# Performance work log

Hardware: AMD Instinct MI355X
Metric: run time of the kernel (lower is better)

The kernel has to match this reference:

```python
import jax, jax.numpy as jnp
import numpy as np

B, S, D = 8, 2048, 768
H = 4 * D  # MLP hidden
EPS = 1e-5


def setup_inputs() -> dict:
    key = jax.random.key(0)
    ks = jax.random.split(key, 12)
    sd = 1.0 / np.sqrt(D)
    sh = 1.0 / np.sqrt(H)
    return {
        "x": jax.random.normal(ks[0], (B, S, D), dtype=jnp.float32),
        "ln1_g": jnp.ones((D,), jnp.float32),
        "ln1_b": jnp.zeros((D,), jnp.float32),
        "ln2_g": jnp.ones((D,), jnp.float32),
        "ln2_b": jnp.zeros((D,), jnp.float32),
        "Wq": jax.random.normal(ks[1], (D, D), jnp.float32) * sd,
        "bq": jnp.zeros((D,), jnp.float32),
        "Wk": jax.random.normal(ks[2], (D, D), jnp.float32) * sd,
        "bk": jnp.zeros((D,), jnp.float32),
        "Wv": jax.random.normal(ks[3], (D, D), jnp.float32) * sd,
        "bv": jnp.zeros((D,), jnp.float32),
        "Wo": jax.random.normal(ks[4], (D, D), jnp.float32) * sd,
        "bo": jnp.zeros((D,), jnp.float32),
        "Wfc": jax.random.normal(ks[5], (D, H), jnp.float32) * sd,
        "bfc": jnp.zeros((H,), jnp.float32),
        "Wproj": jax.random.normal(ks[6], (H, D), jnp.float32) * sh,
        "bproj": jnp.zeros((D,), jnp.float32),
    }


def _layernorm(x, g, b):
    mu = jnp.mean(x, axis=-1, keepdims=True)
    var = jnp.mean(jnp.square(x - mu), axis=-1, keepdims=True)
    return (x - mu) * jax.lax.rsqrt(var + EPS) * g + b


def reference(x, ln1_g, ln1_b, ln2_g, ln2_b, Wq, bq, Wk, bk, Wv, bv, Wo, bo,
              Wfc, bfc, Wproj, bproj):
    d = x.shape[-1]
    # --- attention sub-block (single head, full D) ---
    h = _layernorm(x, ln1_g, ln1_b)
    q = h @ Wq + bq            # [B,S,D]
    k = h @ Wk + bk
    v = h @ Wv + bv
    scores = jnp.einsum("bsd,btd->bst", q, k) / jnp.sqrt(jnp.float32(d))
    attn = jax.nn.softmax(scores, axis=-1)  # softmax over keys (dim=2)
    y = jnp.einsum("bst,btd->bsd", attn, v)
    x = x + (y @ Wo + bo)
    # --- MLP sub-block (exact GELU like nn.GELU default) ---
    h2 = _layernorm(x, ln2_g, ln2_b)
    m = jax.nn.gelu(h2 @ Wfc + bfc, approximate=False)
    x = x + (m @ Wproj + bproj)  # dropout p=0 -> identity
    return x
```

## Files before the change

### kernel.cpp

```cpp
#include <hip/hip_runtime.h>
#include <hip/hip_bf16.h>

typedef __attribute__((ext_vector_type(8))) short short8;
typedef __attribute__((ext_vector_type(4))) float floatx4;

using bf16 = __hip_bfloat16;

__device__ __forceinline__ void cp16_g2l(bf16* lds_p, const bf16* g) {
  __builtin_amdgcn_global_load_lds(
      (const __attribute__((address_space(1))) unsigned int*)g,
      (__attribute__((address_space(3))) unsigned int*)lds_p,
      16, 0, 0);
}

__device__ __forceinline__ float gelu_exact(float x) {
  return 0.5f * x * (1.0f + erff(x * 0.70710678118654752f));
}

template<int MODE>
__global__ __launch_bounds__(256)
void gemm_bt(const bf16* __restrict__ A, long sAb, long lda,
             const bf16* __restrict__ Bt, long sBb, long ldb,
             const float* __restrict__ bias,
             const float* __restrict__ resid,
             float* __restrict__ rsum, long rsS, long cbStr,
             void* __restrict__ out, long sOb,
             int N, int K, float scale)
{
  constexpr bool PA = (MODE == 5);

  __shared__ __attribute__((aligned(16))) bf16 sA[3][128 * 32];
  __shared__ __attribute__((aligned(16))) bf16 sB[3][128 * 32];

  const int tid = threadIdx.x;
  const int l = tid & 63, w = tid >> 6;
  const int bz = blockIdx.z;
  const long row0 = (long)blockIdx.x * 128;
  const long col0 = (long)blockIdx.y * 128;

  const bf16* Ab = A + (long)bz * sAb;
  const bf16* Bb = Bt + (long)bz * sBb;

  const int sr = (w << 4) + (l >> 2);
  const int slot = (l & 3) ^ ((sr >> 1) & 3);
  const int kcd = (l & 3) << 3;
  const bf16* gA;
  long skipA, koA;
  if constexpr (PA) {
    gA    = Ab + ((long)(slot >> 1) * lda + row0 + sr) * 16 + ((slot & 1) << 3);
    skipA = 64 * 16;
    koA   = 32 * lda;
  } else {
    gA    = Ab + (row0 + sr) * lda + (slot << 3);
    skipA = 64 * lda;
    koA   = 32;
  }
  const bf16* gB = Bb + (col0 + sr) * ldb + (slot << 3);
  const long skipB = 64 * ldb;
  const int lofs = sr * 32 + kcd;

  floatx4 acc[4][4];
  #pragma unroll
  for (int i = 0; i < 4; ++i)
    #pragma unroll
    for (int j = 0; j < 4; ++j)
      acc[i][j] = (floatx4){0.f, 0.f, 0.f, 0.f};

  const int wr = (w >> 1) & 1, wc = w & 1;
  const int g = l >> 4, t = l & 15;
  const int swz = (g ^ ((t >> 1) & 3)) << 3;
  const int aoff = (wr * 64 + t) * 32 + swz;
  const int boff = (wc * 64 + t) * 32 + swz;

  const int nt = K >> 5;

  cp16_g2l(&sA[0][lofs],           gA);
  cp16_g2l(&sA[0][lofs] + 64 * 32, gA + skipA);
  cp16_g2l(&sB[0][lofs],           gB);
  cp16_g2l(&sB[0][lofs] + 64 * 32, gB + skipB);

  int bufc = 0;
  for (int kt = 0; kt < nt; ++kt) {
    const int nxtb = (bufc == 2) ? 0 : bufc + 1;
    if (kt + 1 < nt) {
      const long oA = (long)(kt + 1) * koA;
      const long oB = (long)(kt + 1) << 5;
      cp16_g2l(&sA[nxtb][lofs],           gA + oA);
      cp16_g2l(&sA[nxtb][lofs] + 64 * 32, gA + oA + skipA);
      cp16_g2l(&sB[nxtb][lofs],           gB + oB);
      cp16_g2l(&sB[nxtb][lofs] + 64 * 32, gB + oB + skipB);
      asm volatile("s_waitcnt vmcnt(4)" ::: "memory");
    } else {
      asm volatile("s_waitcnt vmcnt(0)" ::: "memory");
    }
    asm volatile("s_barrier" ::: "memory");

    const bf16* cA = &sA[bufc][0];
    const bf16* cB = &sB[bufc][0];
    short8 a[4], b[4];
    #pragma unroll
    for (int m = 0; m < 4; ++m) a[m] = *(const short8*)(cA + aoff + m * 512);
    #pragma unroll
    for (int n = 0; n < 4; ++n) b[n] = *(const short8*)(cB + boff + n * 512);
    #pragma unroll
    for (int m = 0; m < 4; ++m)
      #pragma unroll
      for (int n = 0; n < 4; ++n)
        acc[m][n] = __builtin_amdgcn_mfma_f32_16x16x32_bf16(a[m], b[n], acc[m][n], 0, 0, 0);
    bufc = nxtb;
  }

  const long orow = row0 + wr * 64 + (g << 2);
  const long ocol = col0 + wc * 64 + t;

  if constexpr (MODE == 0 || MODE == 4) {
    bf16* O = (bf16*)out + (long)bz * sOb;
    float bv4[4];
    #pragma unroll
    for (int n = 0; n < 4; ++n) bv4[n] = bias[ocol + n * 16];
    #pragma unroll
    for (int m = 0; m < 4; ++m) {
      #pragma unroll
      for (int r = 0; r < 4; ++r) {
        bf16* Or = O + (orow + m * 16 + r) * (long)N + ocol;
        #pragma unroll
        for (int n = 0; n < 4; ++n) {
          float vv = acc[m][n][r] + bv4[n];
          if constexpr (MODE == 4) vv = gelu_exact(vv);
          Or[n * 16] = __float2bfloat16(vv);
        }
      }
    }
  } else if constexpr (MODE == 3) {
    float* O = (float*)out;
    float bv4[4];
    #pragma unroll
    for (int n = 0; n < 4; ++n) bv4[n] = bias[ocol + n * 16];
    #pragma unroll
    for (int m = 0; m < 4; ++m) {
      #pragma unroll
      for (int r = 0; r < 4; ++r) {
        const long rb = (orow + m * 16 + r) * (long)N + ocol;
        #pragma unroll
        for (int n = 0; n < 4; ++n)
          O[rb + n * 16] = acc[m][n][r] + bv4[n] + resid[rb + n * 16];
      }
    }
  } else if constexpr (MODE == 5) {
    bf16* O = (bf16*)out + (long)bz * sOb;
    #pragma unroll
    for (int m = 0; m < 4; ++m) {
      #pragma unroll
      for (int r = 0; r < 4; ++r) {
        const long rr = orow + m * 16 + r;
        const float inv = 1.0f / rsum[bz * rsS + rr];
        bf16* Or = O + rr * (long)N + ocol;
        #pragma unroll
        for (int n = 0; n < 4; ++n)
          Or[n * 16] = __float2bfloat16(acc[m][n][r] * inv);
      }
    }
  } else {
    bf16* O = (bf16*)out + (long)bz * sOb;
    const long pb = (col0 >> 4) + wc * 4;
    float prow[4][4];
    #pragma unroll
    for (int m = 0; m < 4; ++m)
      #pragma unroll
      for (int r = 0; r < 4; ++r) prow[m][r] = 0.f;
    #pragma unroll
    for (int n = 0; n < 4; ++n) {
      bf16* Opan = O + (pb + n) * (rsS * 16) + t;
      #pragma unroll
      for (int m = 0; m < 4; ++m) {
        #pragma unroll
        for (int r = 0; r < 4; ++r) {
          const float p = __expf(acc[m][n][r] * scale);
          Opan[(orow + m * 16 + r) * 16] = __float2bfloat16(p);
          prow[m][r] += p;
        }
      }
    }
    #pragma unroll
    for (int m = 0; m < 4; ++m) {
      #pragma unroll
      for (int r = 0; r < 4; ++r) {
        float s = prow[m][r];
        s += __shfl_xor(s, 1);
        s += __shfl_xor(s, 2);
        s += __shfl_xor(s, 4);
        s += __shfl_xor(s, 8);
        if (t == 0)
          rsum[(long)(blockIdx.y * 2 + wc) * cbStr + bz * rsS +
               orow + m * 16 + r] = s;
      }
    }
  }
}

__global__ __launch_bounds__(256)
void reduce32(const float* __restrict__ rp, float* __restrict__ rs, int n)
{
  const int i = threadIdx.x + blockIdx.x * 256;
  if (i < n) {
    float s = 0.f;
    #pragma unroll
    for (int c = 0; c < 32; ++c) s += rp[(long)c * 16384 + i];
    rs[i] = s;
  }
}

__global__ __launch_bounds__(256)
void ln_kernel(const float* __restrict__ X, const float* __restrict__ G,
               const float* __restrict__ Bv, bf16* __restrict__ H)
{
  const int tid = threadIdx.x;
  const long row = blockIdx.x;
  const float* xr = X + row * 768;
  const float v0 = xr[tid], v1 = xr[tid + 256], v2 = xr[tid + 512];
  float s = v0 + v1 + v2;
  float s2 = v0 * v0 + v1 * v1 + v2 * v2;
  #pragma unroll
  for (int o = 32; o > 0; o >>= 1) {
    s += __shfl_xor(s, o);
    s2 += __shfl_xor(s2, o);
  }
  __shared__ float red[8];
  const int w = tid >> 6, l = tid & 63;
  if (l == 0) { red[w] = s; red[w + 4] = s2; }
  __syncthreads();
  s = red[0] + red[1] + red[2] + red[3];
  s2 = red[4] + red[5] + red[6] + red[7];
  const float mu = s * (1.f / 768.f);
  const float var = s2 * (1.f / 768.f) - mu * mu;
  const float rstd = rsqrtf(var + 1e-5f);
  bf16* hr = H + row * 768;
  hr[tid]       = __float2bfloat16((v0 - mu) * rstd * G[tid]       + Bv[tid]);
  hr[tid + 256] = __float2bfloat16((v1 - mu) * rstd * G[tid + 256] + Bv[tid + 256]);
  hr[tid + 512] = __float2bfloat16((v2 - mu) * rstd * G[tid + 512] + Bv[tid + 512]);
}

__global__ void transpose_w(const float* __restrict__ W, bf16* __restrict__ Wt,
                            int K, int N)
{
  __shared__ float tile[32][33];
  const int n0 = blockIdx.x * 32, k0 = blockIdx.y * 32;
  const int tx = threadIdx.x, ty = threadIdx.y;
  #pragma unroll
  for (int j = ty; j < 32; j += 8)
    tile[j][tx] = W[(long)(k0 + j) * N + n0 + tx];
  __syncthreads();
  #pragma unroll
  for (int j = ty; j < 32; j += 8)
    Wt[(long)(n0 + j) * K + k0 + tx] = __float2bfloat16(tile[tx][j]);
}

__global__ void transpose_v(const bf16* __restrict__ QKV, bf16* __restrict__ Vt)
{
  __shared__ bf16 tile[32][33];
  const int d0 = blockIdx.x * 32, s0 = blockIdx.y * 32, b = blockIdx.z;
  const int tx = threadIdx.x, ty = threadIdx.y;
  #pragma unroll
  for (int j = ty; j < 32; j += 8)
    tile[j][tx] = QKV[((long)b * 2048 + s0 + j) * 2304 + 1536 + d0 + tx];
  __syncthreads();
  #pragma unroll
  for (int j = ty; j < 32; j += 8)
    Vt[(long)b * 768 * 2048 + (long)(d0 + j) * 2048 + s0 + tx] = tile[tx][j];
}

__global__ void concat3(const float* __restrict__ a, const float* __restrict__ b,
                        const float* __restrict__ c, float* __restrict__ o)
{
  const int i = threadIdx.x + blockIdx.x * 256;
  if (i < 768) { o[i] = a[i]; o[i + 768] = b[i]; o[i + 1536] = c[i]; }
}

extern "C" void kernel_launch(void* const* d_in, const int* in_sizes, int n_in,
                              void* d_out, int out_size, void* d_ws, size_t ws_size,
                              hipStream_t stream)
{
  const float* x     = (const float*)d_in[0];
  const float* ln1g  = (const float*)d_in[1];
  const float* ln1b  = (const float*)d_in[2];
  const float* ln2g  = (const float*)d_in[3];
  const float* ln2b  = (const float*)d_in[4];
  const float* Wq    = (const float*)d_in[5];
  const float* bq    = (const float*)d_in[6];
  const float* Wk    = (const float*)d_in[7];
  const float* bk    = (const float*)d_in[8];
  const float* Wv    = (const float*)d_in[9];
  const float* bvv   = (const float*)d_in[10];
  const float* Wo    = (const float*)d_in[11];
  const float* bo    = (const float*)d_in[12];
  const float* Wfc   = (const float*)d_in[13];
  const float* bfc   = (const float*)d_in[14];
  const float* Wproj = (const float*)d_in[15];
  const float* bproj = (const float*)d_in[16];
  float* out = (float*)d_out;

  constexpr int Bz = 8, S = 2048, D = 768, Hh = 3072, QKVN = 3 * D;
  constexpr long Mtot = (long)Bz * S;

  char* ws = (char*)d_ws;
  size_t off = 0;
  auto alloc = [&](size_t bytes) -> char* {
    char* p = ws + off;
    off += (bytes + 255) & ~(size_t)255;
    return p;
  };
  bf16* wqkvT = (bf16*)alloc((size_t)QKVN * D * 2);
  bf16* woT   = (bf16*)alloc((size_t)D * D * 2);
  bf16* wfcT  = (bf16*)alloc((size_t)Hh * D * 2);
  bf16* wprT  = (bf16*)alloc((size_t)D * Hh * 2);
  float* bqkv = (float*)alloc((size_t)QKVN * 4);
  float* rsum = (float*)alloc((size_t)Mtot * 4);
  float* rpart= (float*)alloc((size_t)32 * Mtot * 4);
  bf16* hb    = (bf16*)alloc((size_t)Mtot * D * 2);
  bf16* qkv   = (bf16*)alloc((size_t)Mtot * QKVN * 2);
  bf16* vtb   = (bf16*)alloc((size_t)Mtot * D * 2);
  bf16* yb    = (bf16*)alloc((size_t)Mtot * D * 2);

  int nbat = Bz;
  size_t region = (size_t)nbat * S * S * 2;
  const size_t mbytes = (size_t)Mtot * Hh * 2;
  if (region < mbytes) region = mbytes;
  if (off + region > ws_size) {
    nbat = 1;
    region = mbytes;
  }
  char* reg = alloc(region);
  bf16* attn = (bf16*)reg;
  bf16* mb = (bf16*)reg;

  const dim3 tb(32, 8);

  transpose_w<<<dim3(D / 32, D / 32), tb, 0, stream>>>(Wq, wqkvT, D, D);
  transpose_w<<<dim3(D / 32, D / 32), tb, 0, stream>>>(Wk, wqkvT + (size_t)D * D, D, D);
  transpose_w<<<dim3(D / 32, D / 32), tb, 0, stream>>>(Wv, wqkvT + 2 * (size_t)D * D, D, D);
  transpose_w<<<dim3(D / 32, D / 32), tb, 0, stream>>>(Wo, woT, D, D);
  transpose_w<<<dim3(Hh / 32, D / 32), tb, 0, stream>>>(Wfc, wfcT, D, Hh);
  transpose_w<<<dim3(D / 32, Hh / 32), tb, 0, stream>>>(Wproj, wprT, Hh, D);
  concat3<<<3, 256, 0, stream>>>(bq, bk, bvv, bqkv);

  ln_kernel<<<(int)Mtot, 256, 0, stream>>>(x, ln1g, ln1b, hb);

  gemm_bt<0><<<dim3(Mtot / 128, QKVN / 128, 1), 256, 0, stream>>>(
      hb, 0, D, wqkvT, 0, D, bqkv, nullptr, nullptr, 0, 0, qkv, 0, QKVN, D, 1.f);
  transpose_v<<<dim3(D / 32, S / 32, Bz), tb, 0, stream>>>(qkv, vtb);

  const float sc = 0.03608439182435161f;
  for (int g0 = 0; g0 < Bz; g0 += nbat) {
    const bf16* qg  = qkv + (long)g0 * S * QKVN;
    const bf16* kg  = qkv + (long)g0 * S * QKVN + D;
    const bf16* vtg = vtb + (long)g0 * D * S;
    float* rsg = rsum + (long)g0 * S;
    float* rpg = rpart + (long)g0 * S;
    bf16* yg = yb + (long)g0 * S * D;
    gemm_bt<6><<<dim3(S / 128, S / 128, nbat), 256, 0, stream>>>(
        qg, (long)S * QKVN, QKVN, kg, (long)S * QKVN, QKVN, nullptr, nullptr,
        rpg, S, Mtot, attn, (long)S * S, S, D, sc);
    reduce32<<<(int)(Mtot / 256), 256, 0, stream>>>(rpart, rsum, (int)Mtot);
    gemm_bt<5><<<dim3(S / 128, D / 128, nbat), 256, 0, stream>>>(
        attn, (long)S * S, S, vtg, (long)D * S, S, nullptr, nullptr,
        rsg, S, 0, yg, (long)S * D, D, S, 1.f);
  }

  gemm_bt<3><<<dim3(Mtot / 128, D / 128, 1), 256, 0, stream>>>(
      yb, 0, D, woT, 0, D, bo, x, nullptr, 0, 0, out, 0, D, D, 1.f);

  ln_kernel<<<(int)Mtot, 256, 0, stream>>>(out, ln2g, ln2b, hb);

  gemm_bt<4><<<dim3(Mtot / 128, Hh / 128, 1), 256, 0, stream>>>(
      hb, 0, D, wfcT, 0, D, bfc, nullptr, nullptr, 0, 0, mb, 0, Hh, D, 1.f);
  gemm_bt<3><<<dim3(Mtot / 128, D / 128, 1), 256, 0, stream>>>(
      mb, 0, Hh, wprT, 0, Hh, bproj, out, nullptr, 0, 0, out, 0, D, Hh, 1.f);
}
```

Measured before the change: 625.6 us.

## Compute softmax row sums via ones-MFMA, remap workgroups, store residual in bf16

The PV GEMM now computes the softmax denominators itself by running an extra MFMA of the probability tile against a ones vector. This removes the partial-sum writes in the QK kernel and the separate reduce32 launch. Workgroup IDs are remapped with an XCD-aware interleave to improve L2 locality across chiplets. The intermediate residual x1 is stored in bf16, reusing the qkv buffer, and read back by a new bf16 layernorm and the final GEMM. This halves that traffic but loses precision in the residual stream.

```diff
diff --git a/kernel.cpp b/kernel.cpp
--- a/kernel.cpp
+++ b/kernel.cpp
@@ -22,21 +22,29 @@
 void gemm_bt(const bf16* __restrict__ A, long sAb, long lda,
              const bf16* __restrict__ Bt, long sBb, long ldb,
              const float* __restrict__ bias,
-             const float* __restrict__ resid,
-             float* __restrict__ rsum, long rsS, long cbStr,
+             const float* __restrict__ residf,
+             const bf16* __restrict__ residb,
              void* __restrict__ out, long sOb,
              int N, int K, float scale)
 {
-  constexpr bool PA = (MODE == 5);
+  constexpr bool PA   = (MODE == 5);
+  constexpr bool ONES = (MODE == 5);
 
   __shared__ __attribute__((aligned(16))) bf16 sA[3][128 * 32];
   __shared__ __attribute__((aligned(16))) bf16 sB[3][128 * 32];
 
+  const int nwg = gridDim.x * gridDim.y * gridDim.z;
+  int lid = blockIdx.x + gridDim.x * (blockIdx.y + gridDim.y * blockIdx.z);
+  lid = (lid & 7) * (nwg >> 3) + (lid >> 3);
+  const int bx = lid % gridDim.x;
+  const int tmp = lid / gridDim.x;
+  const int by = tmp % gridDim.y;
+  const int bz = tmp / gridDim.y;
+
   const int tid = threadIdx.x;
   const int l = tid & 63, w = tid >> 6;
-  const int bz = blockIdx.z;
-  const long row0 = (long)blockIdx.x * 128;
-  const long col0 = (long)blockIdx.y * 128;
+  const long row0 = (long)bx * 128;
+  const long col0 = (long)by * 128;
 
   const bf16* Ab = A + (long)bz * sAb;
   const bf16* Bb = Bt + (long)bz * sBb;
@@ -65,6 +73,11 @@
     #pragma unroll
     for (int j = 0; j < 4; ++j)
       acc[i][j] = (floatx4){0.f, 0.f, 0.f, 0.f};
+  floatx4 accs[4];
+  #pragma unroll
+  for (int i = 0; i < 4; ++i) accs[i] = (floatx4){0.f, 0.f, 0.f, 0.f};
+  const short8 b_ones = {0x3F80, 0x3F80, 0x3F80, 0x3F80,
+                         0x3F80, 0x3F80, 0x3F80, 0x3F80};
 
   const int wr = (w >> 1) & 1, wc = w & 1;
   const int g = l >> 4, t = l & 15;
@@ -107,6 +120,11 @@
       #pragma unroll
       for (int n = 0; n < 4; ++n)
         acc[m][n] = __builtin_amdgcn_mfma_f32_16x16x32_bf16(a[m], b[n], acc[m][n], 0, 0, 0);
+    if constexpr (ONES) {
+      #pragma unroll
+      for (int m = 0; m < 4; ++m)
+        accs[m] = __builtin_amdgcn_mfma_f32_16x16x32_bf16(a[m], b_ones, accs[m], 0, 0, 0);
+    }
     bufc = nxtb;
   }
 
@@ -131,8 +149,8 @@
         }
       }
     }
-  } else if constexpr (MODE == 3) {
-    float* O = (float*)out;
+  } else if constexpr (MODE == 7) {
+    bf16* O = (bf16*)out;
     float bv4[4];
     #pragma unroll
     for (int n = 0; n < 4; ++n) bv4[n] = bias[ocol + n * 16];
@@ -143,7 +161,24 @@
         const long rb = (orow + m * 16 + r) * (long)N + ocol;
         #pragma unroll
         for (int n = 0; n < 4; ++n)
-          O[rb + n * 16] = acc[m][n][r] + bv4[n] + resid[rb + n * 16];
+          O[rb + n * 16] =
+              __float2bfloat16(acc[m][n][r] + bv4[n] + residf[rb + n * 16]);
+      }
+    }
+  } else if constexpr (MODE == 8) {
+    float* O = (float*)out;
+    float bv4[4];
+    #pragma unroll
+    for (int n = 0; n < 4; ++n) bv4[n] = bias[ocol + n * 16];
+    #pragma unroll
+    for (int m = 0; m < 4; ++m) {
+      #pragma unroll
+      for (int r = 0; r < 4; ++r) {
+        const long rb = (orow + m * 16 + r) * (long)N + ocol;
+        #pragma unroll
+        for (int n = 0; n < 4; ++n)
+          O[rb + n * 16] = acc[m][n][r] + bv4[n] +
+                           __bfloat162float(residb[rb + n * 16]);
       }
     }
   } else if constexpr (MODE == 5) {
@@ -153,7 +188,7 @@
       #pragma unroll
       for (int r = 0; r < 4; ++r) {
         const long rr = orow + m * 16 + r;
-        const float inv = 1.0f / rsum[bz * rsS + rr];
+        const float inv = 1.0f / accs[m][r];
         bf16* Or = O + rr * (long)N + ocol;
         #pragma unroll
         for (int n = 0; n < 4; ++n)
@@ -163,50 +198,17 @@
   } else {
     bf16* O = (bf16*)out + (long)bz * sOb;
     const long pb = (col0 >> 4) + wc * 4;
-    float prow[4][4];
-    #pragma unroll
-    for (int m = 0; m < 4; ++m)
-      #pragma unroll
-      for (int r = 0; r < 4; ++r) prow[m][r] = 0.f;
     #pragma unroll
     for (int n = 0; n < 4; ++n) {
-      bf16* Opan = O + (pb + n) * (rsS * 16) + t;
+      bf16* Opan = O + (pb + n) * ((long)N * 16) + t;
       #pragma unroll
       for (int m = 0; m < 4; ++m) {
         #pragma unroll
-        for (int r = 0; r < 4; ++r) {
-          const float p = __expf(acc[m][n][r] * scale);
-          Opan[(orow + m * 16 + r) * 16] = __float2bfloat16(p);
-          prow[m][r] += p;
-        }
+        for (int r = 0; r < 4; ++r)
+          Opan[(orow + m * 16 + r) * 16] =
+              __float2bfloat16(__expf(acc[m][n][r] * scale));
       }
     }
-    #pragma unroll
-    for (int m = 0; m < 4; ++m) {
-      #pragma unroll
-      for (int r = 0; r < 4; ++r) {
-        float s = prow[m][r];
-        s += __shfl_xor(s, 1);
-        s += __shfl_xor(s, 2);
-        s += __shfl_xor(s, 4);
-        s += __shfl_xor(s, 8);
-        if (t == 0)
-          rsum[(long)(blockIdx.y * 2 + wc) * cbStr + bz * rsS +
-               orow + m * 16 + r] = s;
-      }
-    }
-  }
-}
-
-__global__ __launch_bounds__(256)
-void reduce32(const float* __restrict__ rp, float* __restrict__ rs, int n)
-{
-  const int i = threadIdx.x + blockIdx.x * 256;
-  if (i < n) {
-    float s = 0.f;
-    #pragma unroll
-    for (int c = 0; c < 32; ++c) s += rp[(long)c * 16384 + i];
-    rs[i] = s;
   }
 }
 
@@ -218,6 +220,38 @@
   const long row = blockIdx.x;
   const float* xr = X + row * 768;
   const float v0 = xr[tid], v1 = xr[tid + 256], v2 = xr[tid + 512];
+  float s = v0 + v1 + v2;
+  float s2 = v0 * v0 + v1 * v1 + v2 * v2;
+  #pragma unroll
+  for (int o = 32; o > 0; o >>= 1) {
+    s += __shfl_xor(s, o);
+    s2 += __shfl_xor(s2, o);
+  }
+  __shared__ float red[8];
+  const int w = tid >> 6, l = tid & 63;
+  if (l == 0) { red[w] = s; red[w + 4] = s2; }
+  __syncthreads();
+  s = red[0] + red[1] + red[2] + red[3];
+  s2 = red[4] + red[5] + red[6] + red[7];
+  const float mu = s * (1.f / 768.f);
+  const float var = s2 * (1.f / 768.f) - mu * mu;
+  const float rstd = rsqrtf(var + 1e-5f);
+  bf16* hr = H + row * 768;
+  hr[tid]       = __float2bfloat16((v0 - mu) * rstd * G[tid]       + Bv[tid]);
+  hr[tid + 256] = __float2bfloat16((v1 - mu) * rstd * G[tid + 256] + Bv[tid + 256]);
+  hr[tid + 512] = __float2bfloat16((v2 - mu) * rstd * G[tid + 512] + Bv[tid + 512]);
+}
+
+__global__ __launch_bounds__(256)
+void lnb_kernel(const bf16* __restrict__ X, const float* __restrict__ G,
+                const float* __restrict__ Bv, bf16* __restrict__ H)
+{
+  const int tid = threadIdx.x;
+  const long row = blockIdx.x;
+  const bf16* xr = X + row * 768;
+  const float v0 = __bfloat162float(xr[tid]);
+  const float v1 = __bfloat162float(xr[tid + 256]);
+  const float v2 = __bfloat162float(xr[tid + 512]);
   float s = v0 + v1 + v2;
   float s2 = v0 * v0 + v1 * v1 + v2 * v2;
   #pragma unroll
@@ -314,12 +348,11 @@
   bf16* wfcT  = (bf16*)alloc((size_t)Hh * D * 2);
   bf16* wprT  = (bf16*)alloc((size_t)D * Hh * 2);
   float* bqkv = (float*)alloc((size_t)QKVN * 4);
-  float* rsum = (float*)alloc((size_t)Mtot * 4);
-  float* rpart= (float*)alloc((size_t)32 * Mtot * 4);
   bf16* hb    = (bf16*)alloc((size_t)Mtot * D * 2);
   bf16* qkv   = (bf16*)alloc((size_t)Mtot * QKVN * 2);
   bf16* vtb   = (bf16*)alloc((size_t)Mtot * D * 2);
   bf16* yb    = (bf16*)alloc((size_t)Mtot * D * 2);
+  bf16* x1b = qkv;
 
   int nbat = Bz;
   size_t region = (size_t)nbat * S * S * 2;
@@ -346,7 +379,7 @@
   ln_kernel<<<(int)Mtot, 256, 0, stream>>>(x, ln1g, ln1b, hb);
 
   gemm_bt<0><<<dim3(Mtot / 128, QKVN / 128, 1), 256, 0, stream>>>(
-      hb, 0, D, wqkvT, 0, D, bqkv, nullptr, nullptr, 0, 0, qkv, 0, QKVN, D, 1.f);
+      hb, 0, D, wqkvT, 0, D, bqkv, nullptr, nullptr, qkv, 0, QKVN, D, 1.f);
   transpose_v<<<dim3(D / 32, S / 32, Bz), tb, 0, stream>>>(qkv, vtb);
 
   const float sc = 0.03608439182435161f;
@@ -354,25 +387,22 @@
     const bf16* qg  = qkv + (long)g0 * S * QKVN;
     const bf16* kg  = qkv + (long)g0 * S * QKVN + D;
     const bf16* vtg = vtb + (long)g0 * D * S;
-    float* rsg = rsum + (long)g0 * S;
-    float* rpg = rpart + (long)g0 * S;
     bf16* yg = yb + (long)g0 * S * D;
     gemm_bt<6><<<dim3(S / 128, S / 128, nbat), 256, 0, stream>>>(
         qg, (long)S * QKVN, QKVN, kg, (long)S * QKVN, QKVN, nullptr, nullptr,
-        rpg, S, Mtot, attn, (long)S * S, S, D, sc);
-    reduce32<<<(int)(Mtot / 256), 256, 0, stream>>>(rpart, rsum, (int)Mtot);
+        nullptr, attn, (long)S * S, S, D, sc);
     gemm_bt<5><<<dim3(S / 128, D / 128, nbat), 256, 0, stream>>>(
         attn, (long)S * S, S, vtg, (long)D * S, S, nullptr, nullptr,
-        rsg, S, 0, yg, (long)S * D, D, S, 1.f);
-  }
-
-  gemm_bt<3><<<dim3(Mtot / 128, D / 128, 1), 256, 0, stream>>>(
-      yb, 0, D, woT, 0, D, bo, x, nullptr, 0, 0, out, 0, D, D, 1.f);
-
-  ln_kernel<<<(int)Mtot, 256, 0, stream>>>(out, ln2g, ln2b, hb);
+        nullptr, yg, (long)S * D, D, S, 1.f);
+  }
+
+  gemm_bt<7><<<dim3(Mtot / 128, D / 128, 1), 256, 0, stream>>>(
+      yb, 0, D, woT, 0, D, bo, x, nullptr, x1b, 0, D, D, 1.f);
+
+  lnb_kernel<<<(int)Mtot, 256, 0, stream>>>(x1b, ln2g, ln2b, hb);
 
   gemm_bt<4><<<dim3(Mtot / 128, Hh / 128, 1), 256, 0, stream>>>(
-      hb, 0, D, wfcT, 0, D, bfc, nullptr, nullptr, 0, 0, mb, 0, Hh, D, 1.f);
-  gemm_bt<3><<<dim3(Mtot / 128, D / 128, 1), 256, 0, stream>>>(
-      mb, 0, Hh, wprT, 0, Hh, bproj, out, nullptr, 0, 0, out, 0, D, Hh, 1.f);
-}
+      hb, 0, D, wfcT, 0, D, bfc, nullptr, nullptr, mb, 0, Hh, D, 1.f);
+  gemm_bt<8><<<dim3(Mtot / 128, D / 128, 1), 256, 0, stream>>>(
+      mb, 0, Hh, wprT, 0, Hh, bproj, nullptr, x1b, out, 0, D, Hh, 1.f);
+}
```

Result: faster. 611.6 us (-2.2%).
